# Kernel tuning notes

Hardware: AMD Instinct MI355X
Metric: run time of the kernel (lower is better)

## Reference

```python
import jax, jax.numpy as jnp
import numpy as np

N = 50000          # nodes
E = 800000         # edges per view (avg degree 16)
HID = 128
EMB = 64
K = 10
INPUT_DIMS = [1000, 800, 600]


def setup_inputs() -> dict:
    key = jax.random.key(0)
    ks = jax.random.split(key, 32)
    d = {}
    for i, din in enumerate(INPUT_DIMS):
        d[f"x{i}"] = jax.random.normal(ks[i], (N, din), jnp.float32)
        d[f"rows{i}"] = jax.random.randint(ks[3 + i], (E,), 0, N)
        d[f"cols{i}"] = jax.random.randint(ks[6 + i], (E,), 0, N)
        d[f"vals{i}"] = jax.random.uniform(ks[9 + i], (E,), jnp.float32)
        s1 = 1.0 / np.sqrt(HID)   # GraphConvolution.reset_parameters: 1/sqrt(out_features)
        s2 = 1.0 / np.sqrt(EMB)
        d[f"w1_{i}"] = jax.random.uniform(ks[12 + i], (din, HID), jnp.float32, -s1, s1)
        d[f"b1_{i}"] = jax.random.uniform(ks[15 + i], (HID,), jnp.float32, -s1, s1)
        d[f"w2_{i}"] = jax.random.uniform(ks[18 + i], (HID, EMB), jnp.float32, -s2, s2)
        d[f"b2_{i}"] = jax.random.uniform(ks[21 + i], (EMB,), jnp.float32, -s2, s2)
    sf = 1.0 / np.sqrt(EMB * 3)   # nn.Linear default init
    d["fusion_w"] = jax.random.uniform(ks[24], (EMB * 3, EMB), jnp.float32, -sf, sf)
    d["fusion_b"] = jax.random.uniform(ks[25], (EMB,), jnp.float32, -sf, sf)
    xav = np.sqrt(2.0 / (K + EMB))  # xavier_normal_
    d["cluster"] = jax.random.normal(ks[26], (K, EMB), jnp.float32) * xav
    return d


def _spmm(rows, cols, vals, dense):
    # adj (COO, NxN) @ dense [N, F] -> [N, F]
    return jax.ops.segment_sum(vals[:, None] * dense[cols], rows, num_segments=N)


def _encode(x, rows, cols, vals, w1, b1, w2, b2):
    h = jax.nn.relu(_spmm(rows, cols, vals, x @ w1) + b1)
    # F.dropout in eval mode = identity
    return _spmm(rows, cols, vals, h @ w2) + b2


def reference(x0, x1, x2,
              rows0, cols0, vals0,
              rows1, cols1, vals1,
              rows2, cols2, vals2,
              w1_0, b1_0, w2_0, b2_0,
              w1_1, b1_1, w2_1, b2_1,
              w1_2, b1_2, w2_2, b2_2,
              fusion_w, fusion_b, cluster):
    z0 = _encode(x0, rows0, cols0, vals0, w1_0, b1_0, w2_0, b2_0)
    z1 = _encode(x1, rows1, cols1, vals1, w1_1, b1_1, w2_1, b2_1)
    z2 = _encode(x2, rows2, cols2, vals2, w1_2, b1_2, w2_2, b2_2)
    z_concat = jnp.concatenate([z0, z1, z2], axis=1)          # [N, 3*EMB]
    z_fused = jax.nn.relu(z_concat @ fusion_w + fusion_b)     # [N, EMB]
    # DEC-style soft assignment (Student-t, alpha=1 -> exponent (1+1)/2 = 1)
    d2 = jnp.sum((z_fused[:, None, :] - cluster[None, :, :]) ** 2, axis=2)  # [N, K]
    q = 1.0 / (1.0 + d2)
    q = q / jnp.sum(q, axis=1, keepdims=True)
    return (z0, z1, z2, z_fused, q)
```

## Files before the change

### kernel.cpp

```cpp
#include <hip/hip_runtime.h>


#define N_NODES 50000
#define N_EDGES 800000
#define HID 128
#define EMB 64
#define NCLU 10

using bf16x8 = __attribute__((ext_vector_type(8))) short;
using f32x4  = __attribute__((ext_vector_type(4))) float;

static __device__ __forceinline__ unsigned short f2bf(float f) {
    unsigned int u = __float_as_uint(f);
    unsigned int r = (u + 0x7FFF + ((u >> 16) & 1)) >> 16;
    return (unsigned short)r;
}
static __device__ __forceinline__ float bflo(unsigned int t) {
    return __uint_as_float(t << 16);
}
static __device__ __forceinline__ float bfhi(unsigned int t) {
    return __uint_as_float(t & 0xFFFF0000u);
}


__global__ void hist_kernel(const int* __restrict__ rows, int* __restrict__ counts, int E) {
    int t = blockIdx.x * 256 + threadIdx.x;
    if (t < E) atomicAdd(&counts[rows[t]], 1);
}

__global__ __launch_bounds__(256) void scan1_kernel(
    const int* __restrict__ counts, int* __restrict__ tmp, int* __restrict__ bsum, int n)
{
    __shared__ int wt[4];
    int t = threadIdx.x, b = blockIdx.x;
    int i = b * 256 + t;
    int lane = t & 63, wid = t >> 6;
    int v = (i < n) ? counts[i] : 0;
    int incl = v;
    #pragma unroll
    for (int d = 1; d < 64; d <<= 1) {
        int u = __shfl_up(incl, d, 64);
        if (lane >= d) incl += u;
    }
    if (lane == 63) wt[wid] = incl;
    __syncthreads();
    int woff = 0;
    #pragma unroll
    for (int w = 0; w < 4; ++w) if (w < wid) woff += wt[w];
    if (i < n) tmp[i] = woff + incl - v;
    if (t == 255) bsum[b] = woff + incl;
}

__global__ __launch_bounds__(256) void scan2_kernel(
    const int* __restrict__ bsum, int* __restrict__ boff, int nb,
    int* __restrict__ row_ptr, int n)
{
    __shared__ int wt[4];
    int t = threadIdx.x;
    int lane = t & 63, wid = t >> 6;
    int v = (t < nb) ? bsum[t] : 0;
    int incl = v;
    #pragma unroll
    for (int d = 1; d < 64; d <<= 1) {
        int u = __shfl_up(incl, d, 64);
        if (lane >= d) incl += u;
    }
    if (lane == 63) wt[wid] = incl;
    __syncthreads();
    int woff = 0;
    #pragma unroll
    for (int w = 0; w < 4; ++w) if (w < wid) woff += wt[w];
    if (t < nb) boff[t] = woff + incl - v;
    if (t == nb - 1) row_ptr[n] = woff + incl;
}

__global__ __launch_bounds__(256) void scan3_kernel(
    const int* __restrict__ tmp, const int* __restrict__ boff,
    int* __restrict__ row_ptr, int* __restrict__ cursor, int n)
{
    int i = blockIdx.x * 256 + threadIdx.x;
    if (i < n) {
        int e = tmp[i] + boff[blockIdx.x];
        row_ptr[i] = e;
        cursor[i] = e;
    }
}

__global__ void scatter_kernel(const int* __restrict__ rows, const int* __restrict__ cols,
                               const float* __restrict__ vals, int* __restrict__ cursor,
                               float2* __restrict__ cv, int E) {
    int t = blockIdx.x * 256 + threadIdx.x;
    if (t < E) {
        int r = rows[t];
        int p = atomicAdd(&cursor[r], 1);
        float2 e;
        e.x = __uint_as_float((unsigned int)cols[t]);
        e.y = vals[t];
        cv[p] = e;
    }
}


__global__ void wconv_kernel(const float* __restrict__ w, unsigned short* __restrict__ wt,
                             int din, int dinp) {
    int t = blockIdx.x * 256 + threadIdx.x;
    if (t >= 128 * dinp) return;
    int n = t / dinp, k = t - n * dinp;
    float f = (k < din) ? w[(size_t)k * 128 + n] : 0.f;
    wt[(size_t)n * dinp + k] = f2bf(f);
}


#define SA 40

__global__ __launch_bounds__(256) void gemm1_kernel(
    const float* __restrict__ x, const unsigned short* __restrict__ w1t,
    unsigned short* __restrict__ xw, int Nn, int din, int dinp)
{
    __shared__ unsigned short As[128 * SA];
    __shared__ unsigned short Bs[128 * 32];
    int tid = threadIdx.x;
    int lane = tid & 63, wid = tid >> 6;
    int wm = wid & 1, wn = wid >> 1;
    int row0 = blockIdx.x * 128;
    f32x4 acc[4][4] = {};
    int numK = dinp >> 5;
    int sa_k = (tid & 7) * 4;
    int sa_r = tid >> 3;
    for (int kt = 0; kt < numK; ++kt) {
        int k0 = kt << 5;
        __syncthreads();
        #pragma unroll
        for (int p = 0; p < 4; ++p) {
            int r = sa_r + p * 32;
            int gr = row0 + r;
            float4 v = make_float4(0.f, 0.f, 0.f, 0.f);
            if (gr < Nn && (k0 + sa_k) < din)
                v = *(const float4*)(x + (size_t)gr * din + k0 + sa_k);
            ushort4 b;
            b.x = f2bf(v.x); b.y = f2bf(v.y); b.z = f2bf(v.z); b.w = f2bf(v.w);
            *(ushort4*)(&As[r * SA + sa_k]) = b;
        }
        #pragma unroll
        for (int p = 0; p < 2; ++p) {
            int idx = p * 256 + tid;
            int n = idx >> 2, quad = idx & 3;
            bf16x8 t = *(const bf16x8*)(w1t + (size_t)n * dinp + k0 + quad * 8);
            *(bf16x8*)(&Bs[n * 32 + quad * 8]) = t;
        }
        __syncthreads();
        int kq = (lane >> 4) * 8;
        int sub = lane & 15;
        bf16x8 af[4], bfr[4];
        #pragma unroll
        for (int mt = 0; mt < 4; ++mt)
            af[mt] = *(const bf16x8*)(&As[(wm * 64 + mt * 16 + sub) * SA + kq]);
        #pragma unroll
        for (int nt = 0; nt < 4; ++nt)
            bfr[nt] = *(const bf16x8*)(&Bs[(wn * 64 + nt * 16 + sub) * 32 + kq]);
        #pragma unroll
        for (int mt = 0; mt < 4; ++mt)
            #pragma unroll
            for (int nt = 0; nt < 4; ++nt)
                acc[mt][nt] = __builtin_amdgcn_mfma_f32_16x16x32_bf16(af[mt], bfr[nt], acc[mt][nt], 0, 0, 0);
    }
    #pragma unroll
    for (int mt = 0; mt < 4; ++mt) {
        #pragma unroll
        for (int nt = 0; nt < 4; ++nt) {
            int col = wn * 64 + nt * 16 + (lane & 15);
            #pragma unroll
            for (int r = 0; r < 4; ++r) {
                int row = row0 + wm * 64 + mt * 16 + (lane >> 4) * 4 + r;
                if (row < Nn) xw[(size_t)row * 128 + col] = f2bf(acc[mt][nt][r]);
            }
        }
    }
}


__global__ __launch_bounds__(256) void spmm128_kernel(
    const unsigned short* __restrict__ src, const int* __restrict__ row_ptr,
    const float2* __restrict__ cv, const float* __restrict__ bias,
    unsigned short* __restrict__ dst)
{
    const unsigned int* srcu = (const unsigned int*)src;
    int lane = threadIdx.x & 63;
    int r = blockIdx.x * 4 + (threadIdx.x >> 6);
    int s = row_ptr[r], e = row_ptr[r + 1];
    float a0 = 0.f, a1 = 0.f, b0 = 0.f, b1 = 0.f;
    int j = s;
    for (; j + 4 <= e; j += 4) {
        float2 p0 = cv[j], p1 = cv[j + 1], p2 = cv[j + 2], p3 = cv[j + 3];
        unsigned int t0 = srcu[(size_t)__float_as_uint(p0.x) * 64 + lane];
        unsigned int t1 = srcu[(size_t)__float_as_uint(p1.x) * 64 + lane];
        unsigned int t2 = srcu[(size_t)__float_as_uint(p2.x) * 64 + lane];
        unsigned int t3 = srcu[(size_t)__float_as_uint(p3.x) * 64 + lane];
        a0 += p0.y * bflo(t0); a1 += p0.y * bfhi(t0);
        b0 += p1.y * bflo(t1); b1 += p1.y * bfhi(t1);
        a0 += p2.y * bflo(t2); a1 += p2.y * bfhi(t2);
        b0 += p3.y * bflo(t3); b1 += p3.y * bfhi(t3);
    }
    for (; j < e; ++j) {
        float2 p = cv[j];
        unsigned int t = srcu[(size_t)__float_as_uint(p.x) * 64 + lane];
        a0 += p.y * bflo(t); a1 += p.y * bfhi(t);
    }
    a0 += b0 + bias[lane * 2];
    a1 += b1 + bias[lane * 2 + 1];
    a0 = fmaxf(a0, 0.f); a1 = fmaxf(a1, 0.f);
    unsigned int o = (unsigned int)f2bf(a0) | ((unsigned int)f2bf(a1) << 16);
    ((unsigned int*)dst)[(size_t)r * 64 + lane] = o;
}


__global__ __launch_bounds__(256) void spmm64_kernel(
    const unsigned short* __restrict__ src, const int* __restrict__ row_ptr,
    const float2* __restrict__ cv, const float* __restrict__ bias,
    float* __restrict__ dst)
{
    int lane = threadIdx.x & 63;
    int r = blockIdx.x * 4 + (threadIdx.x >> 6);
    int s = row_ptr[r], e = row_ptr[r + 1];
    float a0 = 0.f, b0 = 0.f;
    int j = s;
    for (; j + 4 <= e; j += 4) {
        float2 p0 = cv[j], p1 = cv[j + 1], p2 = cv[j + 2], p3 = cv[j + 3];
        float f0 = __uint_as_float((unsigned int)src[(size_t)__float_as_uint(p0.x) * 64 + lane] << 16);
        float f1 = __uint_as_float((unsigned int)src[(size_t)__float_as_uint(p1.x) * 64 + lane] << 16);
        float f2 = __uint_as_float((unsigned int)src[(size_t)__float_as_uint(p2.x) * 64 + lane] << 16);
        float f3 = __uint_as_float((unsigned int)src[(size_t)__float_as_uint(p3.x) * 64 + lane] << 16);
        a0 += p0.y * f0; b0 += p1.y * f1;
        a0 += p2.y * f2; b0 += p3.y * f3;
    }
    for (; j < e; ++j) {
        float2 p = cv[j];
        float f = __uint_as_float((unsigned int)src[(size_t)__float_as_uint(p.x) * 64 + lane] << 16);
        a0 += p.y * f;
    }
    dst[(size_t)r * 64 + lane] = a0 + b0 + bias[lane];
}


__global__ __launch_bounds__(256) void gemm2_kernel(
    const unsigned short* __restrict__ h, const float* __restrict__ w2,
    unsigned short* __restrict__ hw)
{
    __shared__ float w2s[128 * 64];
    int tid = threadIdx.x;
    for (int i = tid; i < 128 * 64; i += 256) w2s[i] = w2[i];
    __syncthreads();
    int n = tid & 63, g = tid >> 6;
    int r0 = blockIdx.x * 16 + g * 4;
    const unsigned int* h0 = (const unsigned int*)(h + (size_t)r0 * 128);
    float a0 = 0.f, a1 = 0.f, a2 = 0.f, a3 = 0.f;
    #pragma unroll 4
    for (int k2 = 0; k2 < 64; ++k2) {
        unsigned int t0 = h0[k2], t1 = h0[64 + k2], t2 = h0[128 + k2], t3 = h0[192 + k2];
        float w0 = w2s[(2 * k2) * 64 + n];
        float w1 = w2s[(2 * k2 + 1) * 64 + n];
        a0 += bflo(t0) * w0 + bfhi(t0) * w1;
        a1 += bflo(t1) * w0 + bfhi(t1) * w1;
        a2 += bflo(t2) * w0 + bfhi(t2) * w1;
        a3 += bflo(t3) * w0 + bfhi(t3) * w1;
    }
    hw[(size_t)(r0 + 0) * 64 + n] = f2bf(a0);
    hw[(size_t)(r0 + 1) * 64 + n] = f2bf(a1);
    hw[(size_t)(r0 + 2) * 64 + n] = f2bf(a2);
    hw[(size_t)(r0 + 3) * 64 + n] = f2bf(a3);
}


__global__ __launch_bounds__(256) void fusion_kernel(
    const float* __restrict__ z, const float* __restrict__ fw,
    const float* __restrict__ fb, float* __restrict__ zf)
{
    __shared__ float ws_[192 * 64];
    int tid = threadIdx.x;
    for (int i = tid; i < 192 * 64; i += 256) ws_[i] = fw[i];
    __syncthreads();
    int n = tid & 63, g = tid >> 6;
    int r0 = blockIdx.x * 16 + g * 4;
    float a0 = 0.f, a1 = 0.f, a2 = 0.f, a3 = 0.f;
    #pragma unroll
    for (int v = 0; v < 3; ++v) {
        const float* zv = z + (size_t)v * N_NODES * 64;
        const float* z0 = zv + (size_t)(r0 + 0) * 64;
        const float* z1 = zv + (size_t)(r0 + 1) * 64;
        const float* z2 = zv + (size_t)(r0 + 2) * 64;
        const float* z3 = zv + (size_t)(r0 + 3) * 64;
        #pragma unroll 4
        for (int k = 0; k < 64; ++k) {
            float w = ws_[(v * 64 + k) * 64 + n];
            a0 += z0[k] * w; a1 += z1[k] * w; a2 += z2[k] * w; a3 += z3[k] * w;
        }
    }
    float b = fb[n];
    zf[(size_t)(r0 + 0) * 64 + n] = fmaxf(a0 + b, 0.f);
    zf[(size_t)(r0 + 1) * 64 + n] = fmaxf(a1 + b, 0.f);
    zf[(size_t)(r0 + 2) * 64 + n] = fmaxf(a2 + b, 0.f);
    zf[(size_t)(r0 + 3) * 64 + n] = fmaxf(a3 + b, 0.f);
}


__global__ __launch_bounds__(256) void q_kernel(
    const float* __restrict__ zf, const float* __restrict__ cluster, float* __restrict__ q)
{
    int lane = threadIdx.x & 63;
    int r = blockIdx.x * 4 + (threadIdx.x >> 6);
    float zl = zf[(size_t)r * 64 + lane];
    float d2[NCLU];
    #pragma unroll
    for (int k = 0; k < NCLU; ++k) {
        float d = zl - cluster[k * 64 + lane];
        float s = d * d;
        #pragma unroll
        for (int m = 32; m; m >>= 1) s += __shfl_xor(s, m, 64);
        d2[k] = s;
    }
    float S = 0.f;
    #pragma unroll
    for (int k = 0; k < NCLU; ++k) S += 1.f / (1.f + d2[k]);
    float myq = 0.f;
    #pragma unroll
    for (int k = 0; k < NCLU; ++k)
        if (lane == k) myq = 1.f / (1.f + d2[k]);
    if (lane < NCLU) q[(size_t)r * NCLU + lane] = myq / S;
}


extern "C" void kernel_launch(void* const* d_in, const int* in_sizes, int n_in,
                              void* d_out, int out_size, void* d_ws, size_t ws_size,
                              hipStream_t stream)
{
    const int N = N_NODES, E = N_EDGES;
    const int NB = (N + 255) / 256;
    static const int dins[3] = {1000, 800, 600};
    float* out = (float*)d_out;
    char* base = (char*)d_ws;
    size_t off = 0;
    auto alloc = [&](size_t bytes) -> void* {
        void* p = base + off;
        off = (off + bytes + 255) & ~(size_t)255;
        return p;
    };
    unsigned short* xw = (unsigned short*)alloc((size_t)N * 128 * 2);
    unsigned short* h  = (unsigned short*)alloc((size_t)N * 128 * 2);
    unsigned short* hw = (unsigned short*)alloc((size_t)N * 64 * 2);
    unsigned short* w1t = (unsigned short*)alloc(128 * 1024 * 2);
    int* counts  = (int*)alloc((size_t)N * 4);
    int* cursor  = (int*)alloc((size_t)N * 4);
    int* row_ptr = (int*)alloc((size_t)(N + 1) * 4);
    int* tmp     = (int*)alloc((size_t)N * 4);
    int* bsum    = (int*)alloc((size_t)NB * 4);
    int* boff    = (int*)alloc((size_t)NB * 4);
    float2* cv   = (float2*)alloc((size_t)E * 8);

    for (int v = 0; v < 3; ++v) {
        const float* x    = (const float*)d_in[8 * v + 0];
        const int*   rows = (const int*)  d_in[8 * v + 1];
        const int*   cols = (const int*)  d_in[8 * v + 2];
        const float* vals = (const float*)d_in[8 * v + 3];
        const float* w1   = (const float*)d_in[8 * v + 4];
        const float* b1   = (const float*)d_in[8 * v + 5];
        const float* w2   = (const float*)d_in[8 * v + 6];
        const float* b2   = (const float*)d_in[8 * v + 7];
        int din = dins[v], dinp = (din + 31) & ~31;

        hipMemsetAsync(counts, 0, (size_t)N * 4, stream);
        hist_kernel<<<E / 256, 256, 0, stream>>>(rows, counts, E);
        scan1_kernel<<<NB, 256, 0, stream>>>(counts, tmp, bsum, N);
        scan2_kernel<<<1, 256, 0, stream>>>(bsum, boff, NB, row_ptr, N);
        scan3_kernel<<<NB, 256, 0, stream>>>(tmp, boff, row_ptr, cursor, N);
        scatter_kernel<<<E / 256, 256, 0, stream>>>(rows, cols, vals, cursor, cv, E);
        wconv_kernel<<<(128 * dinp + 255) / 256, 256, 0, stream>>>(w1, w1t, din, dinp);
        gemm1_kernel<<<(N + 127) / 128, 256, 0, stream>>>(x, w1t, xw, N, din, dinp);
        spmm128_kernel<<<N / 4, 256, 0, stream>>>(xw, row_ptr, cv, b1, h);
        gemm2_kernel<<<N / 16, 256, 0, stream>>>(h, w2, hw);
        spmm64_kernel<<<N / 4, 256, 0, stream>>>(hw, row_ptr, cv, b2,
                                                 out + (size_t)v * N * 64);
    }
    const float* fw = (const float*)d_in[24];
    const float* fb = (const float*)d_in[25];
    const float* cl = (const float*)d_in[26];
    fusion_kernel<<<N / 16, 256, 0, stream>>>(out, fw, fb, out + (size_t)3 * N * 64);
    q_kernel<<<N / 4, 256, 0, stream>>>(out + (size_t)3 * N * 64, cl, out + (size_t)4 * N * 64);
}
```

Before: 1.339 ms.

## Batch CSR build across views, pipeline gemm1 with register prefetch, unroll SpMM

```diff
diff --git a/kernel.cpp b/kernel.cpp
--- a/kernel.cpp
+++ b/kernel.cpp
@@ -23,9 +23,13 @@
 }
 
 
-__global__ void hist_kernel(const int* __restrict__ rows, int* __restrict__ counts, int E) {
+__global__ void hist3_kernel(const int* __restrict__ r0, const int* __restrict__ r1,
+                             const int* __restrict__ r2, int* __restrict__ counts) {
     int t = blockIdx.x * 256 + threadIdx.x;
-    if (t < E) atomicAdd(&counts[rows[t]], 1);
+    int view = t / N_EDGES;
+    int i = t - view * N_EDGES;
+    const int* rp = (view == 0) ? r0 : (view == 1) ? r1 : r2;
+    atomicAdd(&counts[view * N_NODES + rp[i]], 1);
 }
 
 __global__ __launch_bounds__(256) void scan1_kernel(
@@ -58,20 +62,27 @@
     __shared__ int wt[4];
     int t = threadIdx.x;
     int lane = t & 63, wid = t >> 6;
-    int v = (t < nb) ? bsum[t] : 0;
-    int incl = v;
-    #pragma unroll
-    for (int d = 1; d < 64; d <<= 1) {
-        int u = __shfl_up(incl, d, 64);
-        if (lane >= d) incl += u;
-    }
-    if (lane == 63) wt[wid] = incl;
-    __syncthreads();
-    int woff = 0;
-    #pragma unroll
-    for (int w = 0; w < 4; ++w) if (w < wid) woff += wt[w];
-    if (t < nb) boff[t] = woff + incl - v;
-    if (t == nb - 1) row_ptr[n] = woff + incl;
+    int carry = 0;
+    for (int c0 = 0; c0 < nb; c0 += 256) {
+        int i = c0 + t;
+        int v = (i < nb) ? bsum[i] : 0;
+        int incl = v;
+        #pragma unroll
+        for (int d = 1; d < 64; d <<= 1) {
+            int u = __shfl_up(incl, d, 64);
+            if (lane >= d) incl += u;
+        }
+        __syncthreads();
+        if (lane == 63) wt[wid] = incl;
+        __syncthreads();
+        int woff = 0;
+        #pragma unroll
+        for (int w = 0; w < 4; ++w) if (w < wid) woff += wt[w];
+        int chunktot = wt[0] + wt[1] + wt[2] + wt[3];
+        if (i < nb) boff[i] = carry + woff + incl - v;
+        carry += chunktot;
+    }
+    if (t == 0) row_ptr[n] = carry;
 }
 
 __global__ __launch_bounds__(256) void scan3_kernel(
@@ -86,18 +97,24 @@
     }
 }
 
-__global__ void scatter_kernel(const int* __restrict__ rows, const int* __restrict__ cols,
-                               const float* __restrict__ vals, int* __restrict__ cursor,
-                               float2* __restrict__ cv, int E) {
+__global__ void scatter3_kernel(
+    const int* __restrict__ r0, const int* __restrict__ c0, const float* __restrict__ v0,
+    const int* __restrict__ r1, const int* __restrict__ c1, const float* __restrict__ v1,
+    const int* __restrict__ r2, const int* __restrict__ c2, const float* __restrict__ v2,
+    int* __restrict__ cursor, float2* __restrict__ cv)
+{
     int t = blockIdx.x * 256 + threadIdx.x;
-    if (t < E) {
-        int r = rows[t];
-        int p = atomicAdd(&cursor[r], 1);
-        float2 e;
-        e.x = __uint_as_float((unsigned int)cols[t]);
-        e.y = vals[t];
-        cv[p] = e;
-    }
+    int view = t / N_EDGES;
+    int i = t - view * N_EDGES;
+    const int* rp = (view == 0) ? r0 : (view == 1) ? r1 : r2;
+    const int* cp = (view == 0) ? c0 : (view == 1) ? c1 : c2;
+    const float* vp = (view == 0) ? v0 : (view == 1) ? v1 : v2;
+    int r = view * N_NODES + rp[i];
+    int p = atomicAdd(&cursor[r], 1);
+    float2 e;
+    e.x = __uint_as_float((unsigned int)cp[i]);
+    e.y = vp[i];
+    cv[p] = e;
 }
 
 
@@ -111,67 +128,109 @@
 }
 
 
-#define SA 40
+#define SAW 72
 
 __global__ __launch_bounds__(256) void gemm1_kernel(
     const float* __restrict__ x, const unsigned short* __restrict__ w1t,
     unsigned short* __restrict__ xw, int Nn, int din, int dinp)
 {
-    __shared__ unsigned short As[128 * SA];
-    __shared__ unsigned short Bs[128 * 32];
+    __shared__ unsigned short As[64 * SAW];
+    __shared__ unsigned short Bs[128 * SAW];
     int tid = threadIdx.x;
     int lane = tid & 63, wid = tid >> 6;
-    int wm = wid & 1, wn = wid >> 1;
-    int row0 = blockIdx.x * 128;
-    f32x4 acc[4][4] = {};
-    int numK = dinp >> 5;
-    int sa_k = (tid & 7) * 4;
-    int sa_r = tid >> 3;
-    for (int kt = 0; kt < numK; ++kt) {
-        int k0 = kt << 5;
+    int row0 = blockIdx.x * 64;
+    int numK = dinp >> 6;
+
+    int ar = tid >> 4;
+    int ak = (tid & 15) * 4;
+    float4 apre[4];
+    uint4  bpre[4];
+
+    auto loadA = [&](int k0) {
+        #pragma unroll
+        for (int p = 0; p < 4; ++p) {
+            int r = p * 16 + ar;
+            int gr = row0 + r;
+            int k = k0 + ak;
+            float4 v = make_float4(0.f, 0.f, 0.f, 0.f);
+            if (gr < Nn) {
+                if (k + 4 <= din) {
+                    v = *(const float4*)(x + (size_t)gr * din + k);
+                } else {
+                    float e0 = (k + 0 < din) ? x[(size_t)gr * din + k + 0] : 0.f;
+                    float e1 = (k + 1 < din) ? x[(size_t)gr * din + k + 1] : 0.f;
+                    float e2 = (k + 2 < din) ? x[(size_t)gr * din + k + 2] : 0.f;
+                    float e3 = (k + 3 < din) ? x[(size_t)gr * din + k + 3] : 0.f;
+                    v = make_float4(e0, e1, e2, e3);
+                }
+            }
+            apre[p] = v;
+        }
+    };
+    auto loadB = [&](int k0) {
+        #pragma unroll
+        for (int p = 0; p < 4; ++p) {
+            int idx = p * 256 + tid;
+            int n = idx >> 3, q = idx & 7;
+            bpre[p] = *(const uint4*)(w1t + (size_t)n * dinp + k0 + q * 8);
+        }
+    };
+    auto storeLDS = [&]() {
+        #pragma unroll
+        for (int p = 0; p < 4; ++p) {
+            int r = p * 16 + ar;
+            ushort4 b;
+            b.x = f2bf(apre[p].x); b.y = f2bf(apre[p].y);
+            b.z = f2bf(apre[p].z); b.w = f2bf(apre[p].w);
+            *(ushort4*)(&As[r * SAW + ak]) = b;
+        }
+        #pragma unroll
+        for (int p = 0; p < 4; ++p) {
+            int idx = p * 256 + tid;
+            int n = idx >> 3, q = idx & 7;
+            *(uint4*)(&Bs[n * SAW + q * 8]) = bpre[p];
+        }
+    };
+
+    loadA(0); loadB(0);
+    storeLDS();
+
+    int kq = (lane >> 4) * 8;
+    int sub = lane & 15;
+    f32x4 acc[4][2] = {};
+    for (int kt = 0;;) {
         __syncthreads();
-        #pragma unroll
-        for (int p = 0; p < 4; ++p) {
-            int r = sa_r + p * 32;
-            int gr = row0 + r;
-            float4 v = make_float4(0.f, 0.f, 0.f, 0.f);
-            if (gr < Nn && (k0 + sa_k) < din)
-                v = *(const float4*)(x + (size_t)gr * din + k0 + sa_k);
-            ushort4 b;
-            b.x = f2bf(v.x); b.y = f2bf(v.y); b.z = f2bf(v.z); b.w = f2bf(v.w);
-            *(ushort4*)(&As[r * SA + sa_k]) = b;
-        }
-        #pragma unroll
-        for (int p = 0; p < 2; ++p) {
-            int idx = p * 256 + tid;
-            int n = idx >> 2, quad = idx & 3;
-            bf16x8 t = *(const bf16x8*)(w1t + (size_t)n * dinp + k0 + quad * 8);
-            *(bf16x8*)(&Bs[n * 32 + quad * 8]) = t;
-        }
+        bool more = (kt + 1 < numK);
+        if (more) { loadA((kt + 1) << 6); loadB((kt + 1) << 6); }
+        #pragma unroll
+        for (int kh = 0; kh < 2; ++kh) {
+            bf16x8 af[4], bfr[2];
+            #pragma unroll
+            for (int mt = 0; mt < 4; ++mt)
+                af[mt] = *(const bf16x8*)(&As[(mt * 16 + sub) * SAW + kh * 32 + kq]);
+            #pragma unroll
+            for (int nt = 0; nt < 2; ++nt)
+                bfr[nt] = *(const bf16x8*)(&Bs[(wid * 32 + nt * 16 + sub) * SAW + kh * 32 + kq]);
+            #pragma unroll
+            for (int mt = 0; mt < 4; ++mt)
+                #pragma unroll
+                for (int nt = 0; nt < 2; ++nt)
+                    acc[mt][nt] = __builtin_amdgcn_mfma_f32_16x16x32_bf16(af[mt], bfr[nt], acc[mt][nt], 0, 0, 0);
+        }
+        if (!more) break;
         __syncthreads();
-        int kq = (lane >> 4) * 8;
-        int sub = lane & 15;
-        bf16x8 af[4], bfr[4];
-        #pragma unroll
-        for (int mt = 0; mt < 4; ++mt)
-            af[mt] = *(const bf16x8*)(&As[(wm * 64 + mt * 16 + sub) * SA + kq]);
-        #pragma unroll
-        for (int nt = 0; nt < 4; ++nt)
-            bfr[nt] = *(const bf16x8*)(&Bs[(wn * 64 + nt * 16 + sub) * 32 + kq]);
-        #pragma unroll
-        for (int mt = 0; mt < 4; ++mt)
-            #pragma unroll
-            for (int nt = 0; nt < 4; ++nt)
-                acc[mt][nt] = __builtin_amdgcn_mfma_f32_16x16x32_bf16(af[mt], bfr[nt], acc[mt][nt], 0, 0, 0);
-    }
+        storeLDS();
+        ++kt;
+    }
+
     #pragma unroll
     for (int mt = 0; mt < 4; ++mt) {
         #pragma unroll
-        for (int nt = 0; nt < 4; ++nt) {
-            int col = wn * 64 + nt * 16 + (lane & 15);
+        for (int nt = 0; nt < 2; ++nt) {
+            int col = wid * 32 + nt * 16 + (lane & 15);
             #pragma unroll
             for (int r = 0; r < 4; ++r) {
-                int row = row0 + wm * 64 + mt * 16 + (lane >> 4) * 4 + r;
+                int row = row0 + mt * 16 + (lane >> 4) * 4 + r;
                 if (row < Nn) xw[(size_t)row * 128 + col] = f2bf(acc[mt][nt][r]);
             }
         }
@@ -190,16 +249,25 @@
     int s = row_ptr[r], e = row_ptr[r + 1];
     float a0 = 0.f, a1 = 0.f, b0 = 0.f, b1 = 0.f;
     int j = s;
-    for (; j + 4 <= e; j += 4) {
+    for (; j + 8 <= e; j += 8) {
         float2 p0 = cv[j], p1 = cv[j + 1], p2 = cv[j + 2], p3 = cv[j + 3];
+        float2 p4 = cv[j + 4], p5 = cv[j + 5], p6 = cv[j + 6], p7 = cv[j + 7];
         unsigned int t0 = srcu[(size_t)__float_as_uint(p0.x) * 64 + lane];
         unsigned int t1 = srcu[(size_t)__float_as_uint(p1.x) * 64 + lane];
         unsigned int t2 = srcu[(size_t)__float_as_uint(p2.x) * 64 + lane];
         unsigned int t3 = srcu[(size_t)__float_as_uint(p3.x) * 64 + lane];
+        unsigned int t4 = srcu[(size_t)__float_as_uint(p4.x) * 64 + lane];
+        unsigned int t5 = srcu[(size_t)__float_as_uint(p5.x) * 64 + lane];
+        unsigned int t6 = srcu[(size_t)__float_as_uint(p6.x) * 64 + lane];
+        unsigned int t7 = srcu[(size_t)__float_as_uint(p7.x) * 64 + lane];
         a0 += p0.y * bflo(t0); a1 += p0.y * bfhi(t0);
         b0 += p1.y * bflo(t1); b1 += p1.y * bfhi(t1);
         a0 += p2.y * bflo(t2); a1 += p2.y * bfhi(t2);
         b0 += p3.y * bflo(t3); b1 += p3.y * bfhi(t3);
+        a0 += p4.y * bflo(t4); a1 += p4.y * bfhi(t4);
+        b0 += p5.y * bflo(t5); b1 += p5.y * bfhi(t5);
+        a0 += p6.y * bflo(t6); a1 += p6.y * bfhi(t6);
+        b0 += p7.y * bflo(t7); b1 += p7.y * bfhi(t7);
     }
     for (; j < e; ++j) {
         float2 p = cv[j];
@@ -224,14 +292,21 @@
     int s = row_ptr[r], e = row_ptr[r + 1];
     float a0 = 0.f, b0 = 0.f;
     int j = s;
-    for (; j + 4 <= e; j += 4) {
+    for (; j + 8 <= e; j += 8) {
         float2 p0 = cv[j], p1 = cv[j + 1], p2 = cv[j + 2], p3 = cv[j + 3];
+        float2 p4 = cv[j + 4], p5 = cv[j + 5], p6 = cv[j + 6], p7 = cv[j + 7];
         float f0 = __uint_as_float((unsigned int)src[(size_t)__float_as_uint(p0.x) * 64 + lane] << 16);
         float f1 = __uint_as_float((unsigned int)src[(size_t)__float_as_uint(p1.x) * 64 + lane] << 16);
         float f2 = __uint_as_float((unsigned int)src[(size_t)__float_as_uint(p2.x) * 64 + lane] << 16);
         float f3 = __uint_as_float((unsigned int)src[(size_t)__float_as_uint(p3.x) * 64 + lane] << 16);
+        float f4 = __uint_as_float((unsigned int)src[(size_t)__float_as_uint(p4.x) * 64 + lane] << 16);
+        float f5 = __uint_as_float((unsigned int)src[(size_t)__float_as_uint(p5.x) * 64 + lane] << 16);
+        float f6 = __uint_as_float((unsigned int)src[(size_t)__float_as_uint(p6.x) * 64 + lane] << 16);
+        float f7 = __uint_as_float((unsigned int)src[(size_t)__float_as_uint(p7.x) * 64 + lane] << 16);
         a0 += p0.y * f0; b0 += p1.y * f1;
         a0 += p2.y * f2; b0 += p3.y * f3;
+        a0 += p4.y * f4; b0 += p5.y * f5;
+        a0 += p6.y * f6; b0 += p7.y * f7;
     }
     for (; j < e; ++j) {
         float2 p = cv[j];
@@ -334,7 +409,8 @@
                               hipStream_t stream)
 {
     const int N = N_NODES, E = N_EDGES;
-    const int NB = (N + 255) / 256;
+    const int N3 = 3 * N, E3 = 3 * E;
+    const int NB3 = (N3 + 255) / 256;
     static const int dins[3] = {1000, 800, 600};
     float* out = (float*)d_out;
     char* base = (char*)d_ws;
@@ -348,36 +424,46 @@
     unsigned short* h  = (unsigned short*)alloc((size_t)N * 128 * 2);
     unsigned short* hw = (unsigned short*)alloc((size_t)N * 64 * 2);
     unsigned short* w1t = (unsigned short*)alloc(128 * 1024 * 2);
-    int* counts  = (int*)alloc((size_t)N * 4);
-    int* cursor  = (int*)alloc((size_t)N * 4);
-    int* row_ptr = (int*)alloc((size_t)(N + 1) * 4);
-    int* tmp     = (int*)alloc((size_t)N * 4);
-    int* bsum    = (int*)alloc((size_t)NB * 4);
-    int* boff    = (int*)alloc((size_t)NB * 4);
-    float2* cv   = (float2*)alloc((size_t)E * 8);
+    int* counts  = (int*)alloc((size_t)N3 * 4);
+    int* cursor  = (int*)alloc((size_t)N3 * 4);
+    int* row_ptr = (int*)alloc((size_t)(N3 + 1) * 4);
+    int* tmp     = (int*)alloc((size_t)N3 * 4);
+    int* bsum    = (int*)alloc((size_t)NB3 * 4);
+    int* boff    = (int*)alloc((size_t)NB3 * 4);
+    float2* cv   = (float2*)alloc((size_t)E3 * 8);
+
+    const int* rows0 = (const int*)d_in[1];
+    const int* cols0 = (const int*)d_in[2];
+    const float* vals0 = (const float*)d_in[3];
+    const int* rows1 = (const int*)d_in[9];
+    const int* cols1 = (const int*)d_in[10];
+    const float* vals1 = (const float*)d_in[11];
+    const int* rows2 = (const int*)d_in[17];
+    const int* cols2 = (const int*)d_in[18];
+    const float* vals2 = (const float*)d_in[19];
+
+    hipMemsetAsync(counts, 0, (size_t)N3 * 4, stream);
+    hist3_kernel<<<E3 / 256, 256, 0, stream>>>(rows0, rows1, rows2, counts);
+    scan1_kernel<<<NB3, 256, 0, stream>>>(counts, tmp, bsum, N3);
+    scan2_kernel<<<1, 256, 0, stream>>>(bsum, boff, NB3, row_ptr, N3);
+    scan3_kernel<<<NB3, 256, 0, stream>>>(tmp, boff, row_ptr, cursor, N3);
+    scatter3_kernel<<<E3 / 256, 256, 0, stream>>>(rows0, cols0, vals0,
+                                                  rows1, cols1, vals1,
+                                                  rows2, cols2, vals2, cursor, cv);
 
     for (int v = 0; v < 3; ++v) {
         const float* x    = (const float*)d_in[8 * v + 0];
-        const int*   rows = (const int*)  d_in[8 * v + 1];
-        const int*   cols = (const int*)  d_in[8 * v + 2];
-        const float* vals = (const float*)d_in[8 * v + 3];
         const float* w1   = (const float*)d_in[8 * v + 4];
         const float* b1   = (const float*)d_in[8 * v + 5];
         const float* w2   = (const float*)d_in[8 * v + 6];
         const float* b2   = (const float*)d_in[8 * v + 7];
-        int din = dins[v], dinp = (din + 31) & ~31;
-
-        hipMemsetAsync(counts, 0, (size_t)N * 4, stream);
-        hist_kernel<<<E / 256, 256, 0, stream>>>(rows, counts, E);
-        scan1_kernel<<<NB, 256, 0, stream>>>(counts, tmp, bsum, N);
-        scan2_kernel<<<1, 256, 0, stream>>>(bsum, boff, NB, row_ptr, N);
-        scan3_kernel<<<NB, 256, 0, stream>>>(tmp, boff, row_ptr, cursor, N);
-        scatter_kernel<<<E / 256, 256, 0, stream>>>(rows, cols, vals, cursor, cv, E);
+        int din = dins[v], dinp = (din + 63) & ~63;
+
         wconv_kernel<<<(128 * dinp + 255) / 256, 256, 0, stream>>>(w1, w1t, din, dinp);
-        gemm1_kernel<<<(N + 127) / 128, 256, 0, stream>>>(x, w1t, xw, N, din, dinp);
-        spmm128_kernel<<<N / 4, 256, 0, stream>>>(xw, row_ptr, cv, b1, h);
+        gemm1_kernel<<<(N + 63) / 64, 256, 0, stream>>>(x, w1t, xw, N, din, dinp);
+        spmm128_kernel<<<N / 4, 256, 0, stream>>>(xw, row_ptr + v * N, cv, b1, h);
         gemm2_kernel<<<N / 16, 256, 0, stream>>>(h, w2, hw);
-        spmm64_kernel<<<N / 4, 256, 0, stream>>>(hw, row_ptr, cv, b2,
+        spmm64_kernel<<<N / 4, 256, 0, stream>>>(hw, row_ptr + v * N, cv, b2,
                                                  out + (size_t)v * N * 64);
     }
     const float* fw = (const float*)d_in[24];
```

Measured after the change: 1.417 ms. +5.8%, slower.
